# Kernel optimization log

Hardware: AMD Instinct MI355X
Metric: run time of the kernel (lower is better)

The kernel has to match this reference:

```python
import jax, jax.numpy as jnp
import numpy as np

N = 100000  # number of graph nodes
E = 1600000  # number of edges
EPS = 1e-12  # F.normalize eps


def _l2_normalize(x):
    # F.normalize(x): row-wise L2 normalize with eps clamp
    n = jnp.sqrt(jnp.sum(x * x, axis=1, keepdims=True))
    return x / jnp.maximum(n, EPS)


def setup_inputs() -> dict:
    key = jax.random.key(0)
    ks = jax.random.split(key, 8)
    edges = jax.random.randint(ks[0], (E, 2), 0, N, dtype=jnp.int64 if jax.config.jax_enable_x64 else jnp.int32)
    feat = jax.random.normal(ks[1], (N, 300), dtype=jnp.float32)
    label_idx = jax.random.randint(ks[2], (1000,), 0, N, dtype=jnp.int32)
    # xavier_uniform for weights, zeros for bias (per GraphConv init)
    lim1 = float(np.sqrt(6.0 / (300 + 64)))
    lim2 = float(np.sqrt(6.0 / (64 + 64)))
    w1 = jax.random.uniform(ks[3], (300, 64), jnp.float32, -lim1, lim1)
    b1 = jnp.zeros((64,), jnp.float32)
    w2 = jax.random.uniform(ks[4], (64, 64), jnp.float32, -lim2, lim2)
    b2 = jnp.zeros((64,), jnp.float32)
    return {"edges": edges, "feat": feat, "label_idx": label_idx,
            "w1": w1, "b1": b1, "w2": w2, "b2": b2}


def reference(edges, feat, label_idx, w1, b1, w2, b2):
    # normt_spm(adj, method='in'): transpose adjacency then row-normalize by degree
    # original coo entries are (src=edges[:,0], dst=edges[:,1]); after transpose:
    rows = edges[:, 1]
    cols = edges[:, 0]
    ones = jnp.ones((edges.shape[0],), feat.dtype)
    deg = jax.ops.segment_sum(ones, rows, num_segments=N)  # [N]
    inv_deg = jnp.where(deg > 0, 1.0 / deg, 0.0)

    def spmm(h):
        # (D^-1 A^T) @ h via gather + segment_sum, h: [N, d]
        msg = h[cols] * inv_deg[rows][:, None]  # [E, d]
        return jax.ops.segment_sum(msg, rows, num_segments=N)

    x = feat
    for w, b in ((w1, b1), (w2, b2)):
        # GraphConv: adj @ (x @ w) + b, then LeakyReLU(0.2); dropout inactive (eval)
        x = spmm(x @ w) + b
        x = jax.nn.leaky_relu(x, negative_slope=0.2)
        x = _l2_normalize(x)
    return x[label_idx]
```

## Files before the change

### kernel.cpp

```cpp
#include <hip/hip_runtime.h>

#define N_NODES 100000
#define N_EDGES 1600000
#define FEAT_D 300
#define HID_D 64
#define SCAN_NB 98

__global__ void hist_kernel(const int* __restrict__ edges, int* __restrict__ cnt) {
    int e = blockIdx.x * blockDim.x + threadIdx.x;
    if (e < N_EDGES) atomicAdd(&cnt[edges[2 * e + 1]], 1);
}

__global__ void invdeg_kernel(const int* __restrict__ cnt, float* __restrict__ invdeg) {
    int i = blockIdx.x * blockDim.x + threadIdx.x;
    if (i < N_NODES) {
        int d = cnt[i];
        invdeg[i] = d > 0 ? 1.f / (float)d : 0.f;
    }
}

__global__ void scan1_kernel(const int* __restrict__ cnt, int* __restrict__ rp,
                             int* __restrict__ bsum) {
    __shared__ int sh[256];
    int base = blockIdx.x * 1024 + threadIdx.x * 4;
    int v[4];
    int s = 0;
#pragma unroll
    for (int j = 0; j < 4; ++j) {
        int idx = base + j;
        v[j] = (idx < N_NODES) ? cnt[idx] : 0;
        s += v[j];
    }
    sh[threadIdx.x] = s;
    __syncthreads();
    for (int off = 1; off < 256; off <<= 1) {
        int t = (threadIdx.x >= off) ? sh[threadIdx.x - off] : 0;
        __syncthreads();
        sh[threadIdx.x] += t;
        __syncthreads();
    }
    int excl = sh[threadIdx.x] - s;
    if (threadIdx.x == 255) bsum[blockIdx.x] = sh[255];
#pragma unroll
    for (int j = 0; j < 4; ++j) {
        int idx = base + j;
        if (idx < N_NODES) rp[idx] = excl;
        excl += v[j];
    }
}

__global__ void scan2_kernel(int* __restrict__ bsum, int* __restrict__ rp) {
    if (threadIdx.x == 0 && blockIdx.x == 0) {
        int acc = 0;
        for (int i = 0; i < SCAN_NB; ++i) {
            int t = bsum[i];
            bsum[i] = acc;
            acc += t;
        }
        rp[N_NODES] = acc;
    }
}

__global__ void scan3_kernel(int* __restrict__ rp, const int* __restrict__ bsum) {
    int base = blockIdx.x * 1024 + threadIdx.x * 4;
    int add = bsum[blockIdx.x];
#pragma unroll
    for (int j = 0; j < 4; ++j) {
        int idx = base + j;
        if (idx < N_NODES) rp[idx] += add;
    }
}

__global__ void scatter_kernel(const int* __restrict__ edges, const int* __restrict__ rp,
                               int* __restrict__ cursor, int* __restrict__ csr_col) {
    int e = blockIdx.x * blockDim.x + threadIdx.x;
    if (e < N_EDGES) {
        int row = edges[2 * e + 1];
        int p = rp[row] + atomicAdd(&cursor[row], 1);
        csr_col[p] = edges[2 * e];
    }
}

template <int K, int KC>
__global__ __launch_bounds__(256) void gemm_kernel(const float* __restrict__ x,
                                                   const float* __restrict__ w,
                                                   float* __restrict__ out) {
    constexpr int XSTR = 132;
    __shared__ __align__(16) float xT[KC * XSTR];
    __shared__ __align__(16) float wS[KC * 64];

    const int tid = threadIdx.x;
    const int c8 = (tid & 7) * 8;
    const int r4 = (tid >> 3) * 4;
    const long r0 = (long)blockIdx.x * 128;

    float acc[4][8];
#pragma unroll
    for (int i = 0; i < 4; ++i)
#pragma unroll
        for (int j = 0; j < 8; ++j) acc[i][j] = 0.f;

    for (int k0 = 0; k0 < K; k0 += KC) {
        constexpr int F4R = KC / 4;
        for (int i = tid; i < 128 * F4R; i += 256) {
            int r = i / F4R, m = i % F4R;
            long gr = r0 + r;
            float4 v = make_float4(0.f, 0.f, 0.f, 0.f);
            if (gr < N_NODES) v = *(const float4*)(x + gr * K + k0 + 4 * m);
            xT[(4 * m + 0) * XSTR + r] = v.x;
            xT[(4 * m + 1) * XSTR + r] = v.y;
            xT[(4 * m + 2) * XSTR + r] = v.z;
            xT[(4 * m + 3) * XSTR + r] = v.w;
        }
        for (int i = tid; i < KC * 16; i += 256)
            ((float4*)wS)[i] = ((const float4*)(w + (long)k0 * 64))[i];
        __syncthreads();

#pragma unroll 4
        for (int k = 0; k < KC; ++k) {
            float4 xv = *(const float4*)&xT[k * XSTR + r4];
            float4 wa = *(const float4*)&wS[k * 64 + c8];
            float4 wb = *(const float4*)&wS[k * 64 + c8 + 4];
            const float* xp = &xv.x;
            const float* wap = &wa.x;
            const float* wbp = &wb.x;
#pragma unroll
            for (int i = 0; i < 4; ++i) {
                float xi = xp[i];
#pragma unroll
                for (int j = 0; j < 4; ++j) {
                    acc[i][j] = fmaf(xi, wap[j], acc[i][j]);
                    acc[i][j + 4] = fmaf(xi, wbp[j], acc[i][j + 4]);
                }
            }
        }
        __syncthreads();
    }

#pragma unroll
    for (int i = 0; i < 4; ++i) {
        long gr = r0 + r4 + i;
        if (gr < N_NODES) {
            *(float4*)(out + gr * 64 + c8) =
                make_float4(acc[i][0], acc[i][1], acc[i][2], acc[i][3]);
            *(float4*)(out + gr * 64 + c8 + 4) =
                make_float4(acc[i][4], acc[i][5], acc[i][6], acc[i][7]);
        }
    }
}

__global__ void spmm_fused_kernel(const int* __restrict__ rp, const int* __restrict__ csr_col,
                                  const float* __restrict__ invdeg, const float* __restrict__ h,
                                  const float* __restrict__ b, float* __restrict__ out) {
    int row = blockIdx.x * 4 + (threadIdx.x >> 6);
    int lane = threadIdx.x & 63;
    int s = rp[row], e = rp[row + 1];
    float acc0 = 0.f, acc1 = 0.f;
    int i = s;
    for (; i + 2 <= e; i += 2) {
        int c0 = csr_col[i];
        int c1 = csr_col[i + 1];
        acc0 += h[(long)c0 * 64 + lane];
        acc1 += h[(long)c1 * 64 + lane];
    }
    if (i < e) acc0 += h[(long)csr_col[i] * 64 + lane];
    float v = (acc0 + acc1) * invdeg[row] + b[lane];
    v = v >= 0.f ? v : 0.2f * v;
    float ss = v * v;
#pragma unroll
    for (int off = 32; off > 0; off >>= 1) ss += __shfl_xor(ss, off);
    out[(long)row * 64 + lane] = v / fmaxf(sqrtf(ss), 1e-12f);
}

__global__ void gather_kernel(const float* __restrict__ x, const int* __restrict__ idx,
                              float* __restrict__ out) {
    int i = blockIdx.x * blockDim.x + threadIdx.x;
    if (i < 1000 * 64) {
        int r = i >> 6;
        out[i] = x[(long)idx[r] * 64 + (i & 63)];
    }
}

extern "C" void kernel_launch(void* const* d_in, const int* in_sizes, int n_in,
                              void* d_out, int out_size, void* d_ws, size_t ws_size,
                              hipStream_t stream) {
    const int* edges = (const int*)d_in[0];
    const float* feat = (const float*)d_in[1];
    const int* label_idx = (const int*)d_in[2];
    const float* w1 = (const float*)d_in[3];
    const float* b1 = (const float*)d_in[4];
    const float* w2 = (const float*)d_in[5];
    const float* b2 = (const float*)d_in[6];
    float* out = (float*)d_out;

    int* cnt = (int*)d_ws;
    int* cursor = cnt + 100352;
    int* rp = cursor + 100352;
    int* bsum = rp + 100416;
    float* invdeg = (float*)(bsum + 128);
    int* csr_col = (int*)(invdeg + 100352);
    float* bufA = (float*)(csr_col + 1600000);
    float* bufB = bufA + (long)N_NODES * 64;

    hipMemsetAsync(cnt, 0, 2 * 100352 * sizeof(int), stream);
    hist_kernel<<<(N_EDGES + 255) / 256, 256, 0, stream>>>(edges, cnt);
    invdeg_kernel<<<(N_NODES + 255) / 256, 256, 0, stream>>>(cnt, invdeg);
    scan1_kernel<<<SCAN_NB, 256, 0, stream>>>(cnt, rp, bsum);
    scan2_kernel<<<1, 64, 0, stream>>>(bsum, rp);
    scan3_kernel<<<SCAN_NB, 256, 0, stream>>>(rp, bsum);
    scatter_kernel<<<(N_EDGES + 255) / 256, 256, 0, stream>>>(edges, rp, cursor, csr_col);

    const int gemm_blocks = (N_NODES + 127) / 128;

    gemm_kernel<FEAT_D, 60><<<gemm_blocks, 256, 0, stream>>>(feat, w1, bufA);
    spmm_fused_kernel<<<N_NODES / 4, 256, 0, stream>>>(rp, csr_col, invdeg, bufA, b1, bufB);

    gemm_kernel<HID_D, 64><<<gemm_blocks, 256, 0, stream>>>(bufB, w2, bufA);
    spmm_fused_kernel<<<N_NODES / 4, 256, 0, stream>>>(rp, csr_col, invdeg, bufA, b2, bufB);

    gather_kernel<<<(1000 * 64 + 255) / 256, 256, 0, stream>>>(bufB, label_idx, out);
}
```

Baseline: 636.9 us.

## Register-prefetch GEMM tiles and use float4 edge-parallel gathers in SpMM

The GEMM switches from a transposed shared-memory tile with scalar stores to a row-major padded tile written with float4 stores. The next K-chunk is now prefetched into registers while the current chunk is computed, and rows are assigned with a stride of 32 to cut bank conflicts. The SpMM kernel splits each 64-lane wave into four sub-groups that each handle different edges, gathering float4 of h per lane, then combines them with cross-lane shuffles. This raises memory-level parallelism for the random gathers but adds shuffle reductions, and only one sub-group writes the output.

```diff
diff --git a/kernel.cpp b/kernel.cpp
--- a/kernel.cpp
+++ b/kernel.cpp
@@ -85,13 +85,17 @@
 __global__ __launch_bounds__(256) void gemm_kernel(const float* __restrict__ x,
                                                    const float* __restrict__ w,
                                                    float* __restrict__ out) {
-    constexpr int XSTR = 132;
-    __shared__ __align__(16) float xT[KC * XSTR];
+    constexpr int XP = 68;
+    constexpr int F4R = KC / 4;
+    constexpr int NCH = K / KC;
+    constexpr int NX = (128 * F4R + 255) / 256;
+    constexpr int NW = (KC * 16 + 255) / 256;
+    __shared__ __align__(16) float xS[128 * XP];
     __shared__ __align__(16) float wS[KC * 64];
 
     const int tid = threadIdx.x;
+    const int g = tid >> 3;
     const int c8 = (tid & 7) * 8;
-    const int r4 = (tid >> 3) * 4;
     const long r0 = (long)blockIdx.x * 128;
 
     float acc[4][8];
@@ -100,46 +104,82 @@
 #pragma unroll
         for (int j = 0; j < 8; ++j) acc[i][j] = 0.f;
 
-    for (int k0 = 0; k0 < K; k0 += KC) {
-        constexpr int F4R = KC / 4;
-        for (int i = tid; i < 128 * F4R; i += 256) {
-            int r = i / F4R, m = i % F4R;
-            long gr = r0 + r;
-            float4 v = make_float4(0.f, 0.f, 0.f, 0.f);
-            if (gr < N_NODES) v = *(const float4*)(x + gr * K + k0 + 4 * m);
-            xT[(4 * m + 0) * XSTR + r] = v.x;
-            xT[(4 * m + 1) * XSTR + r] = v.y;
-            xT[(4 * m + 2) * XSTR + r] = v.z;
-            xT[(4 * m + 3) * XSTR + r] = v.w;
-        }
-        for (int i = tid; i < KC * 16; i += 256)
-            ((float4*)wS)[i] = ((const float4*)(w + (long)k0 * 64))[i];
-        __syncthreads();
-
-#pragma unroll 4
-        for (int k = 0; k < KC; ++k) {
-            float4 xv = *(const float4*)&xT[k * XSTR + r4];
-            float4 wa = *(const float4*)&wS[k * 64 + c8];
-            float4 wb = *(const float4*)&wS[k * 64 + c8 + 4];
-            const float* xp = &xv.x;
-            const float* wap = &wa.x;
-            const float* wbp = &wb.x;
-#pragma unroll
-            for (int i = 0; i < 4; ++i) {
-                float xi = xp[i];
-#pragma unroll
-                for (int j = 0; j < 4; ++j) {
-                    acc[i][j] = fmaf(xi, wap[j], acc[i][j]);
-                    acc[i][j + 4] = fmaf(xi, wbp[j], acc[i][j + 4]);
+    float4 pfx[NX];
+    float4 pfw[NW];
+
+    auto issue = [&](int k0) {
+#pragma unroll
+        for (int l = 0; l < NX; ++l) {
+            int i = tid + l * 256;
+            pfx[l] = make_float4(0.f, 0.f, 0.f, 0.f);
+            if (i < 128 * F4R) {
+                int r = i / F4R, m = i % F4R;
+                long gr = r0 + r;
+                if (gr < N_NODES) pfx[l] = *(const float4*)(x + gr * K + k0 + 4 * m);
+            }
+        }
+#pragma unroll
+        for (int l = 0; l < NW; ++l) {
+            int i = tid + l * 256;
+            if (i < KC * 16) pfw[l] = ((const float4*)(w + (long)k0 * 64))[i];
+        }
+    };
+    auto commit = [&]() {
+#pragma unroll
+        for (int l = 0; l < NX; ++l) {
+            int i = tid + l * 256;
+            if (i < 128 * F4R) {
+                int r = i / F4R, m = i % F4R;
+                *(float4*)&xS[r * XP + 4 * m] = pfx[l];
+            }
+        }
+#pragma unroll
+        for (int l = 0; l < NW; ++l) {
+            int i = tid + l * 256;
+            if (i < KC * 16) ((float4*)wS)[i] = pfw[l];
+        }
+    };
+
+    issue(0);
+    commit();
+    __syncthreads();
+
+    for (int c = 0; c < NCH; ++c) {
+        if (c + 1 < NCH) issue((c + 1) * KC);
+#pragma unroll 3
+        for (int k = 0; k < KC; k += 4) {
+            float4 xv[4];
+#pragma unroll
+            for (int i = 0; i < 4; ++i)
+                xv[i] = *(const float4*)&xS[(g + 32 * i) * XP + k];
+#pragma unroll
+            for (int kk = 0; kk < 4; ++kk) {
+                float4 wa = *(const float4*)&wS[(k + kk) * 64 + c8];
+                float4 wb = *(const float4*)&wS[(k + kk) * 64 + c8 + 4];
+#pragma unroll
+                for (int i = 0; i < 4; ++i) {
+                    float xi = ((const float*)&xv[i])[kk];
+                    acc[i][0] = fmaf(xi, wa.x, acc[i][0]);
+                    acc[i][1] = fmaf(xi, wa.y, acc[i][1]);
+                    acc[i][2] = fmaf(xi, wa.z, acc[i][2]);
+                    acc[i][3] = fmaf(xi, wa.w, acc[i][3]);
+                    acc[i][4] = fmaf(xi, wb.x, acc[i][4]);
+                    acc[i][5] = fmaf(xi, wb.y, acc[i][5]);
+                    acc[i][6] = fmaf(xi, wb.z, acc[i][6]);
+                    acc[i][7] = fmaf(xi, wb.w, acc[i][7]);
                 }
             }
         }
         __syncthreads();
+        if (c + 1 < NCH) {
+            commit();
+            __syncthreads();
+        }
     }
 
 #pragma unroll
     for (int i = 0; i < 4; ++i) {
-        long gr = r0 + r4 + i;
+        long gr = r0 + g + 32 * i;
         if (gr < N_NODES) {
             *(float4*)(out + gr * 64 + c8) =
                 make_float4(acc[i][0], acc[i][1], acc[i][2], acc[i][3]);
@@ -154,22 +194,66 @@
                                   const float* __restrict__ b, float* __restrict__ out) {
     int row = blockIdx.x * 4 + (threadIdx.x >> 6);
     int lane = threadIdx.x & 63;
+    int sub = lane >> 4;
+    int f4 = (lane & 15) * 4;
     int s = rp[row], e = rp[row + 1];
-    float acc0 = 0.f, acc1 = 0.f;
-    int i = s;
-    for (; i + 2 <= e; i += 2) {
+
+    float4 acc = make_float4(0.f, 0.f, 0.f, 0.f);
+    int i = s + sub;
+    for (; i + 4 < e; i += 8) {
         int c0 = csr_col[i];
-        int c1 = csr_col[i + 1];
-        acc0 += h[(long)c0 * 64 + lane];
-        acc1 += h[(long)c1 * 64 + lane];
-    }
-    if (i < e) acc0 += h[(long)csr_col[i] * 64 + lane];
-    float v = (acc0 + acc1) * invdeg[row] + b[lane];
-    v = v >= 0.f ? v : 0.2f * v;
-    float ss = v * v;
-#pragma unroll
-    for (int off = 32; off > 0; off >>= 1) ss += __shfl_xor(ss, off);
-    out[(long)row * 64 + lane] = v / fmaxf(sqrtf(ss), 1e-12f);
+        int c1 = csr_col[i + 4];
+        float4 v0 = *(const float4*)(h + (long)c0 * 64 + f4);
+        float4 v1 = *(const float4*)(h + (long)c1 * 64 + f4);
+        acc.x += v0.x + v1.x;
+        acc.y += v0.y + v1.y;
+        acc.z += v0.z + v1.z;
+        acc.w += v0.w + v1.w;
+    }
+    if (i < e) {
+        int c0 = csr_col[i];
+        float4 v0 = *(const float4*)(h + (long)c0 * 64 + f4);
+        acc.x += v0.x;
+        acc.y += v0.y;
+        acc.z += v0.z;
+        acc.w += v0.w;
+    }
+
+    acc.x += __shfl_xor(acc.x, 16);
+    acc.y += __shfl_xor(acc.y, 16);
+    acc.z += __shfl_xor(acc.z, 16);
+    acc.w += __shfl_xor(acc.w, 16);
+    acc.x += __shfl_xor(acc.x, 32);
+    acc.y += __shfl_xor(acc.y, 32);
+    acc.z += __shfl_xor(acc.z, 32);
+    acc.w += __shfl_xor(acc.w, 32);
+
+    float id = invdeg[row];
+    float4 bb = *(const float4*)(b + f4);
+    float4 v;
+    v.x = acc.x * id + bb.x;
+    v.y = acc.y * id + bb.y;
+    v.z = acc.z * id + bb.z;
+    v.w = acc.w * id + bb.w;
+    v.x = v.x >= 0.f ? v.x : 0.2f * v.x;
+    v.y = v.y >= 0.f ? v.y : 0.2f * v.y;
+    v.z = v.z >= 0.f ? v.z : 0.2f * v.z;
+    v.w = v.w >= 0.f ? v.w : 0.2f * v.w;
+
+    float ss = v.x * v.x + v.y * v.y + v.z * v.z + v.w * v.w;
+    ss += __shfl_xor(ss, 1);
+    ss += __shfl_xor(ss, 2);
+    ss += __shfl_xor(ss, 4);
+    ss += __shfl_xor(ss, 8);
+    float inv = 1.f / fmaxf(sqrtf(ss), 1e-12f);
+
+    if (sub == 0) {
+        v.x *= inv;
+        v.y *= inv;
+        v.z *= inv;
+        v.w *= inv;
+        *(float4*)(out + (long)row * 64 + f4) = v;
+    }
 }
 
 __global__ void gather_kernel(const float* __restrict__ x, const int* __restrict__ idx,
```

Measured after the change: 572.0 us. 1.11x faster.
